# Kernel optimization log

Hardware: AMD Instinct MI355X
Metric: run time of the kernel (lower is better)

## Reference

```python
import jax, jax.numpy as jnp
import numpy as np
from jax import lax

N = 50000   # nodes per timestep
T = 8       # timesteps
E = 1600000 # edges per timestep
F_IN = 128
H = 128


def setup_inputs() -> dict:
    key = jax.random.key(0)
    ks = jax.random.split(key, 8)
    s_in = 1.0 / np.sqrt(F_IN)
    s_h = 1.0 / np.sqrt(H)
    return {
        "node_feats": jax.random.normal(ks[0], (T, N, F_IN), dtype=jnp.float32),
        "edges": jax.random.randint(ks[1], (T, 2, E), 0, N, dtype=jnp.int32),
        "W1": jax.random.normal(ks[2], (F_IN, H), dtype=jnp.float32) * s_in,
        "b1": jnp.zeros((H,), dtype=jnp.float32),
        "W2": jax.random.normal(ks[3], (H, H), dtype=jnp.float32) * s_h,
        "b2": jnp.zeros((H,), dtype=jnp.float32),
        "Wih": jax.random.normal(ks[4], (4 * H, H), dtype=jnp.float32) * s_h,
        "Whh": jax.random.normal(ks[5], (4 * H, H), dtype=jnp.float32) * s_h,
        "bih": jnp.zeros((4 * H,), dtype=jnp.float32),
        "bhh": jnp.zeros((4 * H,), dtype=jnp.float32),
    }


def _gcn_conv(x, row, col, W, b):
    # PyG GCNConv: h = x @ W; symmetric norm with self-loops; aggregate; + b
    h = x @ W  # [N, H]
    sl = jnp.arange(N, dtype=row.dtype)
    r = jnp.concatenate([row, sl])  # dest
    c = jnp.concatenate([col, sl])  # src
    deg = jax.ops.segment_sum(jnp.ones_like(r, dtype=h.dtype), r, num_segments=N)
    dinv = jnp.where(deg > 0, lax.rsqrt(deg), 0.0)
    norm = dinv[r] * dinv[c]  # [E+N]
    msg = h[c] * norm[:, None]  # [E+N, H]
    out = jax.ops.segment_sum(msg, r, num_segments=N)
    return out + b


def reference(node_feats, edges, W1, b1, W2, b2, Wih, Whh, bih, bhh):
    def gcn_step(_, xs):
        x, ei = xs
        row, col = ei[0], ei[1]
        x = jax.nn.relu(_gcn_conv(x, row, col, W1, b1))
        x = jax.nn.relu(_gcn_conv(x, row, col, W2, b2))
        return None, x

    _, embs = lax.scan(gcn_step, None, (node_feats, edges))  # [T, N, H]

    # Single-layer LSTM over time; nodes are the batch. Gate order: i, f, g, o.
    b = bih + bhh

    def lstm_step(carry, x_t):
        h, c = carry
        gates = x_t @ Wih.T + h @ Whh.T + b  # [N, 4H]
        i, f, g, o = jnp.split(gates, 4, axis=-1)
        i, f, o = jax.nn.sigmoid(i), jax.nn.sigmoid(f), jax.nn.sigmoid(o)
        g = jnp.tanh(g)
        c = f * c + i * g
        h = o * jnp.tanh(c)
        return (h, c), None

    h0 = jnp.zeros((N, H), dtype=node_feats.dtype)
    (h_last, _), _ = lax.scan(lstm_step, (h0, h0), embs)
    return h_last  # [N, H] == lstm_out[:, -1, :]
```

## Files before the change

### kernel.cpp

```cpp
#include <hip/hip_runtime.h>
#include <hip/hip_bf16.h>

#define NN 50000
#define TT 8
#define EE 1600000

constexpr int SCAN_B = 512;
constexpr int NBLK = (NN + SCAN_B - 1) / SCAN_B;

typedef __attribute__((ext_vector_type(8))) short bf16x8;
typedef __attribute__((ext_vector_type(4))) float f32x4;

__device__ inline unsigned short f2bf(float f) {
  unsigned int u = __float_as_uint(f);
  u += 0x7FFFu + ((u >> 16) & 1u);
  return (unsigned short)(u >> 16);
}
__device__ inline float bf2f(unsigned short h) {
  return __uint_as_float(((unsigned int)h) << 16);
}

__global__ void k_zero4(float4* p, long n4) {
  long i = (long)blockIdx.x * blockDim.x + threadIdx.x;
  if (i < n4) p[i] = make_float4(0.f, 0.f, 0.f, 0.f);
}

__global__ void k_zeroi(int* p, int n) {
  int i = blockIdx.x * blockDim.x + threadIdx.x;
  if (i < n) p[i] = 0;
}

__global__ void k_prep(const float* __restrict__ Wih, const float* __restrict__ Whh,
                       const float* __restrict__ W1, const float* __restrict__ W2,
                       const float* __restrict__ bih, const float* __restrict__ bhh,
                       unsigned short* WihH, unsigned short* WihL,
                       unsigned short* WhhH, unsigned short* WhhL,
                       unsigned short* W1tH, unsigned short* W1tL,
                       unsigned short* W2tH, unsigned short* W2tL, float* bsum) {
  int i = blockIdx.x * 256 + threadIdx.x;
  if (i < 512 * 128) {
    float v = Wih[i];
    unsigned short h = f2bf(v);
    WihH[i] = h; WihL[i] = f2bf(v - bf2f(h));
    v = Whh[i];
    h = f2bf(v);
    WhhH[i] = h; WhhL[i] = f2bf(v - bf2f(h));
  }
  if (i < 128 * 128) {
    int n = i >> 7, k = i & 127;
    float v = W1[(long)k * 128 + n];
    unsigned short h = f2bf(v);
    W1tH[i] = h; W1tL[i] = f2bf(v - bf2f(h));
    v = W2[(long)k * 128 + n];
    h = f2bf(v);
    W2tH[i] = h; W2tL[i] = f2bf(v - bf2f(h));
  }
  if (i < 512) bsum[i] = bih[i] + bhh[i];
}

__global__ void k_count(const int* __restrict__ row, int* __restrict__ deg) {
  int e = blockIdx.x * blockDim.x + threadIdx.x;
  if (e < EE) atomicAdd(&deg[row[e]], 1);
}

__global__ void k_scan1(const int* __restrict__ deg, int* __restrict__ rs, int* __restrict__ bsum) {
  __shared__ int s[SCAN_B];
  int t = threadIdx.x;
  int i = blockIdx.x * SCAN_B + t;
  int v = (i < NN) ? deg[i] : 0;
  s[t] = v;
  __syncthreads();
  for (int off = 1; off < SCAN_B; off <<= 1) {
    int add = (t >= off) ? s[t - off] : 0;
    __syncthreads();
    s[t] += add;
    __syncthreads();
  }
  if (i < NN) rs[i] = s[t] - v;
  if (t == SCAN_B - 1) bsum[blockIdx.x] = s[t];
}

__global__ void k_scan2(int* __restrict__ bsum) {
  __shared__ int s[128];
  int t = threadIdx.x;
  int v = (t < NBLK) ? bsum[t] : 0;
  s[t] = v;
  __syncthreads();
  for (int off = 1; off < 128; off <<= 1) {
    int add = (t >= off) ? s[t - off] : 0;
    __syncthreads();
    s[t] += add;
    __syncthreads();
  }
  if (t < NBLK) bsum[t] = s[t] - v;
}

__global__ void k_scan3(int* __restrict__ rs, const int* __restrict__ bsum, const int* __restrict__ deg,
                        float* __restrict__ dinv, int* __restrict__ cursor) {
  int i = blockIdx.x * blockDim.x + threadIdx.x;
  if (i < NN) {
    int v = rs[i] + bsum[i / SCAN_B];
    rs[i] = v;
    cursor[i] = v;
    dinv[i] = rsqrtf((float)(deg[i] + 1));
  }
  if (i == 0) rs[NN] = EE;
}

__global__ void k_scatter(const int* __restrict__ row, const int* __restrict__ col,
                          int* __restrict__ cursor, int* __restrict__ csr) {
  int e = blockIdx.x * blockDim.x + threadIdx.x;
  if (e < EE) {
    int r = row[e];
    int p = atomicAdd(&cursor[r], 1);
    csr[p] = col[e];
  }
}

#define MF(a, b, c) c = __builtin_amdgcn_mfma_f32_16x16x32_bf16(a, b, c, 0, 0, 0)

template <int AMODE>
__launch_bounds__(256) __global__
void k_gemm_mfma(const float* __restrict__ Af,
                 const unsigned short* __restrict__ Ahb, const unsigned short* __restrict__ Alb,
                 const unsigned short* __restrict__ BtH, const unsigned short* __restrict__ BtL,
                 float* __restrict__ C) {
  int tid = threadIdx.x;
  int wv = tid >> 6;
  int lane = tid & 63;
  int rA = lane & 15;
  int kg = lane >> 4;
  int m0 = blockIdx.x * 128 + wv * 32;
  int j0 = blockIdx.y * 32;
  long ar0 = min(m0 + rA, NN - 1);
  long ar1 = min(m0 + 16 + rA, NN - 1);
  long br0 = j0 + rA;
  long br1 = br0 + 16;
  f32x4 acc00 = {0.f, 0.f, 0.f, 0.f}, acc01 = acc00, acc10 = acc00, acc11 = acc00;
#pragma unroll
  for (int k0 = 0; k0 < 128; k0 += 32) {
    long ks = k0 + kg * 8;
    bf16x8 a0h, a0l, a1h, a1l;
    if constexpr (AMODE == 0) {
      float4 u0 = *(const float4*)(Af + ar0 * 128 + ks);
      float4 u1 = *(const float4*)(Af + ar0 * 128 + ks + 4);
      float4 u2 = *(const float4*)(Af + ar1 * 128 + ks);
      float4 u3 = *(const float4*)(Af + ar1 * 128 + ks + 4);
      float va[8] = {u0.x, u0.y, u0.z, u0.w, u1.x, u1.y, u1.z, u1.w};
      float vb[8] = {u2.x, u2.y, u2.z, u2.w, u3.x, u3.y, u3.z, u3.w};
#pragma unroll
      for (int e = 0; e < 8; e++) {
        unsigned short h = f2bf(va[e]);
        a0h[e] = (short)h; a0l[e] = (short)f2bf(va[e] - bf2f(h));
        unsigned short h2 = f2bf(vb[e]);
        a1h[e] = (short)h2; a1l[e] = (short)f2bf(vb[e] - bf2f(h2));
      }
    } else {
      a0h = *(const bf16x8*)(Ahb + ar0 * 128 + ks);
      a0l = *(const bf16x8*)(Alb + ar0 * 128 + ks);
      a1h = *(const bf16x8*)(Ahb + ar1 * 128 + ks);
      a1l = *(const bf16x8*)(Alb + ar1 * 128 + ks);
    }
    bf16x8 b0h = *(const bf16x8*)(BtH + br0 * 128 + ks);
    bf16x8 b0l = *(const bf16x8*)(BtL + br0 * 128 + ks);
    bf16x8 b1h = *(const bf16x8*)(BtH + br1 * 128 + ks);
    bf16x8 b1l = *(const bf16x8*)(BtL + br1 * 128 + ks);
    MF(a0l, b0h, acc00); MF(a0h, b0l, acc00); MF(a0h, b0h, acc00);
    MF(a0l, b1h, acc01); MF(a0h, b1l, acc01); MF(a0h, b1h, acc01);
    MF(a1l, b0h, acc10); MF(a1h, b0l, acc10); MF(a1h, b0h, acc10);
    MF(a1l, b1h, acc11); MF(a1h, b1l, acc11); MF(a1h, b1h, acc11);
  }
#pragma unroll
  for (int r = 0; r < 4; r++) {
    int row0 = m0 + kg * 4 + r;
    int row1 = row0 + 16;
    if (row0 < NN) {
      C[(long)row0 * 128 + j0 + rA] = acc00[r];
      C[(long)row0 * 128 + j0 + 16 + rA] = acc01[r];
    }
    if (row1 < NN) {
      C[(long)row1 * 128 + j0 + rA] = acc10[r];
      C[(long)row1 * 128 + j0 + 16 + rA] = acc11[r];
    }
  }
}

__launch_bounds__(256) __global__
void k_agg(const float* __restrict__ Hm, const float* __restrict__ dinv,
           const int* __restrict__ rs, const int* __restrict__ csr,
           const float* __restrict__ bias,
           unsigned short* __restrict__ outH, unsigned short* __restrict__ outL) {
  int i = blockIdx.x * 8 + (threadIdx.x >> 5);
  int lane = threadIdx.x & 31;
  if (i >= NN) return;
  float di = dinv[i];
  const float4* H4 = (const float4*)Hm;
  float4 a = H4[(long)i * 32 + lane];
  float sw = di * di;
  float4 acc = {a.x * sw, a.y * sw, a.z * sw, a.w * sw};
  int e0 = rs[i], e1 = rs[i + 1];
  int e = e0;
  for (; e + 2 <= e1; e += 2) {
    int c0 = csr[e], c1 = csr[e + 1];
    float w0 = di * dinv[c0], w1 = di * dinv[c1];
    float4 v0 = H4[(long)c0 * 32 + lane];
    float4 v1 = H4[(long)c1 * 32 + lane];
    acc.x += w0 * v0.x + w1 * v1.x;
    acc.y += w0 * v0.y + w1 * v1.y;
    acc.z += w0 * v0.z + w1 * v1.z;
    acc.w += w0 * v0.w + w1 * v1.w;
  }
  if (e < e1) {
    int c0 = csr[e];
    float w0 = di * dinv[c0];
    float4 v0 = H4[(long)c0 * 32 + lane];
    acc.x += w0 * v0.x; acc.y += w0 * v0.y; acc.z += w0 * v0.z; acc.w += w0 * v0.w;
  }
  float4 b = ((const float4*)bias)[lane];
  float4 v;
  v.x = fmaxf(acc.x + b.x, 0.f);
  v.y = fmaxf(acc.y + b.y, 0.f);
  v.z = fmaxf(acc.z + b.z, 0.f);
  v.w = fmaxf(acc.w + b.w, 0.f);
  ushort4 hh, hl;
  unsigned short h;
  h = f2bf(v.x); hh.x = h; hl.x = f2bf(v.x - bf2f(h));
  h = f2bf(v.y); hh.y = h; hl.y = f2bf(v.y - bf2f(h));
  h = f2bf(v.z); hh.z = h; hl.z = f2bf(v.z - bf2f(h));
  h = f2bf(v.w); hh.w = h; hl.w = f2bf(v.w - bf2f(h));
  ((ushort4*)outH)[(long)i * 32 + lane] = hh;
  ((ushort4*)outL)[(long)i * 32 + lane] = hl;
}

__launch_bounds__(256) __global__
void k_gates_lstm(const unsigned short* __restrict__ Xh, const unsigned short* __restrict__ Xl,
                  const unsigned short* __restrict__ Hh, const unsigned short* __restrict__ Hl,
                  const unsigned short* __restrict__ WihH, const unsigned short* __restrict__ WihL,
                  const unsigned short* __restrict__ WhhH, const unsigned short* __restrict__ WhhL,
                  const float* __restrict__ bsum, float* __restrict__ cst,
                  unsigned short* __restrict__ HoH, unsigned short* __restrict__ HoL,
                  float* __restrict__ out, int last) {
  __shared__ float G[4][32][36];
  int tid = threadIdx.x;
  int wv = tid >> 6;
  int lane = tid & 63;
  int rA = lane & 15;
  int kg = lane >> 4;
  int m0 = blockIdx.x * 32;
  int j0 = blockIdx.y * 32;
  long ar0 = min(m0 + rA, NN - 1);
  long ar1 = min(m0 + 16 + rA, NN - 1);
  long br0 = wv * 128 + j0 + rA;
  long br1 = br0 + 16;
  f32x4 acc00 = {0.f, 0.f, 0.f, 0.f}, acc01 = acc00, acc10 = acc00, acc11 = acc00;

  auto kloop = [&](const unsigned short* Ah, const unsigned short* Al,
                   const unsigned short* Bh, const unsigned short* Bl) {
#pragma unroll
    for (int k0 = 0; k0 < 128; k0 += 32) {
      long ks = k0 + kg * 8;
      bf16x8 a0h = *(const bf16x8*)(Ah + ar0 * 128 + ks);
      bf16x8 a0l = *(const bf16x8*)(Al + ar0 * 128 + ks);
      bf16x8 a1h = *(const bf16x8*)(Ah + ar1 * 128 + ks);
      bf16x8 a1l = *(const bf16x8*)(Al + ar1 * 128 + ks);
      bf16x8 b0h = *(const bf16x8*)(Bh + br0 * 128 + ks);
      bf16x8 b0l = *(const bf16x8*)(Bl + br0 * 128 + ks);
      bf16x8 b1h = *(const bf16x8*)(Bh + br1 * 128 + ks);
      bf16x8 b1l = *(const bf16x8*)(Bl + br1 * 128 + ks);
      MF(a0l, b0h, acc00); MF(a0h, b0l, acc00); MF(a0h, b0h, acc00);
      MF(a0l, b1h, acc01); MF(a0h, b1l, acc01); MF(a0h, b1h, acc01);
      MF(a1l, b0h, acc10); MF(a1h, b0l, acc10); MF(a1h, b0h, acc10);
      MF(a1l, b1h, acc11); MF(a1h, b1l, acc11); MF(a1h, b1h, acc11);
    }
  };
  kloop(Xh, Xl, WihH, WihL);
  kloop(Hh, Hl, WhhH, WhhL);

#pragma unroll
  for (int r = 0; r < 4; r++) {
    G[wv][kg * 4 + r][rA] = acc00[r];
    G[wv][kg * 4 + r][16 + rA] = acc01[r];
    G[wv][16 + kg * 4 + r][rA] = acc10[r];
    G[wv][16 + kg * 4 + r][16 + rA] = acc11[r];
  }
  __syncthreads();

  int pr = tid >> 3;
  int pc = (tid & 7) * 4;
  int row = m0 + pr;
  if (row < NN) {
    float4 vgi = *(float4*)&G[0][pr][pc];
    float4 vgf = *(float4*)&G[1][pr][pc];
    float4 vgg = *(float4*)&G[2][pr][pc];
    float4 vgo = *(float4*)&G[3][pr][pc];
    float4 bsi = *(const float4*)(bsum + j0 + pc);
    float4 bsf = *(const float4*)(bsum + 128 + j0 + pc);
    float4 bsg = *(const float4*)(bsum + 256 + j0 + pc);
    float4 bso = *(const float4*)(bsum + 384 + j0 + pc);
    long off = (long)row * 128 + j0 + pc;
    float4 co = *(const float4*)(cst + off);
    float4 cn, hv;
#define LCOMP(X)                                           \
  {                                                        \
    float iv = 1.f / (1.f + expf(-(vgi.X + bsi.X)));       \
    float fv = 1.f / (1.f + expf(-(vgf.X + bsf.X)));       \
    float gv = tanhf(vgg.X + bsg.X);                       \
    float ov = 1.f / (1.f + expf(-(vgo.X + bso.X)));       \
    float c2 = fv * co.X + iv * gv;                        \
    cn.X = c2;                                             \
    hv.X = ov * tanhf(c2);                                 \
  }
    LCOMP(x) LCOMP(y) LCOMP(z) LCOMP(w)
#undef LCOMP
    *(float4*)(cst + off) = cn;
    ushort4 hh, hl;
    unsigned short h;
    h = f2bf(hv.x); hh.x = h; hl.x = f2bf(hv.x - bf2f(h));
    h = f2bf(hv.y); hh.y = h; hl.y = f2bf(hv.y - bf2f(h));
    h = f2bf(hv.z); hh.z = h; hl.z = f2bf(hv.z - bf2f(h));
    h = f2bf(hv.w); hh.w = h; hl.w = f2bf(hv.w - bf2f(h));
    *(ushort4*)(HoH + off) = hh;
    *(ushort4*)(HoL + off) = hl;
    if (last) *(float4*)(out + off) = hv;
  }
}

extern "C" void kernel_launch(void* const* d_in, const int* in_sizes, int n_in,
                              void* d_out, int out_size, void* d_ws, size_t ws_size,
                              hipStream_t stream) {
  const float* feats = (const float*)d_in[0];
  const int*   edges = (const int*)d_in[1];
  const float* W1    = (const float*)d_in[2];
  const float* b1    = (const float*)d_in[3];
  const float* W2    = (const float*)d_in[4];
  const float* b2    = (const float*)d_in[5];
  const float* Wih   = (const float*)d_in[6];
  const float* Whh   = (const float*)d_in[7];
  const float* bih   = (const float*)d_in[8];
  const float* bhh   = (const float*)d_in[9];
  float* out = (float*)d_out;

  char* w = (char*)d_ws;
  auto alloc = [&](size_t bytes) {
    char* p = w;
    w += (bytes + 255) & ~(size_t)255;
    return p;
  };

  const size_t NB2 = (size_t)NN * 128 * 2;
  const size_t NB4 = (size_t)NN * 128 * 4;

  int*   csr    = (int*)alloc((size_t)EE * 4);
  int*   deg    = (int*)alloc((size_t)NN * 4);
  int*   rs     = (int*)alloc((size_t)(NN + 1) * 4);
  int*   cursor = (int*)alloc((size_t)NN * 4);
  float* dinv   = (float*)alloc((size_t)NN * 4);
  int*   bsumP  = (int*)alloc(512);

  float* bufH  = (float*)alloc(NB4);
  unsigned short* bufXh = (unsigned short*)alloc(NB2);
  unsigned short* bufXl = (unsigned short*)alloc(NB2);
  unsigned short* Xembh = (unsigned short*)alloc(NB2);
  unsigned short* Xembl = (unsigned short*)alloc(NB2);

  char* zr = alloc(NB2 + NB2 + NB4);
  unsigned short* HsAh = (unsigned short*)zr;
  unsigned short* HsAl = (unsigned short*)(zr + NB2);
  float* cstate = (float*)(zr + 2 * NB2);

  unsigned short* HsBh = (unsigned short*)alloc(NB2);
  unsigned short* HsBl = (unsigned short*)alloc(NB2);

  unsigned short* WihH = (unsigned short*)alloc(512 * 128 * 2);
  unsigned short* WihL = (unsigned short*)alloc(512 * 128 * 2);
  unsigned short* WhhH = (unsigned short*)alloc(512 * 128 * 2);
  unsigned short* WhhL = (unsigned short*)alloc(512 * 128 * 2);
  unsigned short* W1tH = (unsigned short*)alloc(128 * 128 * 2);
  unsigned short* W1tL = (unsigned short*)alloc(128 * 128 * 2);
  unsigned short* W2tH = (unsigned short*)alloc(128 * 128 * 2);
  unsigned short* W2tL = (unsigned short*)alloc(128 * 128 * 2);
  float* bsum = (float*)alloc(512 * 4);

  k_prep<<<256, 256, 0, stream>>>(Wih, Whh, W1, W2, bih, bhh,
                                  WihH, WihL, WhhH, WhhL, W1tH, W1tL, W2tH, W2tL, bsum);
  {
    long n4 = (long)(2 * NB2 + NB4) / 16;
    k_zero4<<<(int)((n4 + 255) / 256), 256, 0, stream>>>((float4*)zr, n4);
  }

  for (int t = 0; t < TT; t++) {
    const int* erow = edges + (size_t)t * 2 * EE;
    const int* ecol = erow + EE;
    const float* xt = feats + (size_t)t * NN * 128;

    k_zeroi<<<(NN + 255) / 256, 256, 0, stream>>>(deg, NN);
    k_count<<<EE / 256, 256, 0, stream>>>(erow, deg);
    k_scan1<<<NBLK, SCAN_B, 0, stream>>>(deg, rs, bsumP);
    k_scan2<<<1, 128, 0, stream>>>(bsumP);
    k_scan3<<<(NN + 255) / 256, 256, 0, stream>>>(rs, bsumP, deg, dinv, cursor);
    k_scatter<<<EE / 256, 256, 0, stream>>>(erow, ecol, cursor, csr);

    k_gemm_mfma<0><<<dim3(391, 4), 256, 0, stream>>>(xt, nullptr, nullptr, W1tH, W1tL, bufH);
    k_agg<<<NN / 8, 256, 0, stream>>>(bufH, dinv, rs, csr, b1, bufXh, bufXl);
    k_gemm_mfma<1><<<dim3(391, 4), 256, 0, stream>>>(nullptr, bufXh, bufXl, W2tH, W2tL, bufH);
    k_agg<<<NN / 8, 256, 0, stream>>>(bufH, dinv, rs, csr, b2, Xembh, Xembl);

    const unsigned short *rH, *rL;
    unsigned short *wH, *wL;
    if ((t & 1) == 0) { rH = HsAh; rL = HsAl; wH = HsBh; wL = HsBl; }
    else              { rH = HsBh; rL = HsBl; wH = HsAh; wL = HsAl; }
    k_gates_lstm<<<dim3(1563, 4), 256, 0, stream>>>(
        Xembh, Xembl, rH, rL, WihH, WihL, WhhH, WhhL, bsum, cstate,
        wH, wL, out, (t == TT - 1) ? 1 : 0);
  }
}
```

Before: 5.558 ms.

## Pre-scale GEMM rows by dinv, load A once per block, unroll aggregation

The GEMM kernels now compute the full 128-column output per block. Each wave loads and splits its A rows once instead of once per column tile. The output is pre-multiplied by dinv of the source row, so aggregation becomes an unweighted sum with a single final dinv scale, removing per-edge dinv gathers, and the edge loop is unrolled by four. The LSTM gates kernel likewise keeps the X and H fragments in registers and loops over four column tiles with extra block syncs, at the cost of much higher register pressure and possibly lower occupancy.

Result: faster. 5.082 ms (-8.6%).

```diff
diff --git a/kernel.cpp b/kernel.cpp
--- a/kernel.cpp
+++ b/kernel.cpp
@@ -124,23 +124,20 @@
 void k_gemm_mfma(const float* __restrict__ Af,
                  const unsigned short* __restrict__ Ahb, const unsigned short* __restrict__ Alb,
                  const unsigned short* __restrict__ BtH, const unsigned short* __restrict__ BtL,
-                 float* __restrict__ C) {
+                 const float* __restrict__ dinv, float* __restrict__ C) {
   int tid = threadIdx.x;
   int wv = tid >> 6;
   int lane = tid & 63;
   int rA = lane & 15;
   int kg = lane >> 4;
   int m0 = blockIdx.x * 128 + wv * 32;
-  int j0 = blockIdx.y * 32;
   long ar0 = min(m0 + rA, NN - 1);
   long ar1 = min(m0 + 16 + rA, NN - 1);
-  long br0 = j0 + rA;
-  long br1 = br0 + 16;
-  f32x4 acc00 = {0.f, 0.f, 0.f, 0.f}, acc01 = acc00, acc10 = acc00, acc11 = acc00;
-#pragma unroll
-  for (int k0 = 0; k0 < 128; k0 += 32) {
-    long ks = k0 + kg * 8;
-    bf16x8 a0h, a0l, a1h, a1l;
+
+  bf16x8 a[4][2][2];
+#pragma unroll
+  for (int k0 = 0; k0 < 4; k0++) {
+    long ks = k0 * 32 + kg * 8;
     if constexpr (AMODE == 0) {
       float4 u0 = *(const float4*)(Af + ar0 * 128 + ks);
       float4 u1 = *(const float4*)(Af + ar0 * 128 + ks + 4);
@@ -151,77 +148,100 @@
 #pragma unroll
       for (int e = 0; e < 8; e++) {
         unsigned short h = f2bf(va[e]);
-        a0h[e] = (short)h; a0l[e] = (short)f2bf(va[e] - bf2f(h));
-        unsigned short h2 = f2bf(vb[e]);
-        a1h[e] = (short)h2; a1l[e] = (short)f2bf(vb[e] - bf2f(h2));
+        a[k0][0][0][e] = (short)h; a[k0][0][1][e] = (short)f2bf(va[e] - bf2f(h));
+        h = f2bf(vb[e]);
+        a[k0][1][0][e] = (short)h; a[k0][1][1][e] = (short)f2bf(vb[e] - bf2f(h));
       }
     } else {
-      a0h = *(const bf16x8*)(Ahb + ar0 * 128 + ks);
-      a0l = *(const bf16x8*)(Alb + ar0 * 128 + ks);
-      a1h = *(const bf16x8*)(Ahb + ar1 * 128 + ks);
-      a1l = *(const bf16x8*)(Alb + ar1 * 128 + ks);
-    }
-    bf16x8 b0h = *(const bf16x8*)(BtH + br0 * 128 + ks);
-    bf16x8 b0l = *(const bf16x8*)(BtL + br0 * 128 + ks);
-    bf16x8 b1h = *(const bf16x8*)(BtH + br1 * 128 + ks);
-    bf16x8 b1l = *(const bf16x8*)(BtL + br1 * 128 + ks);
-    MF(a0l, b0h, acc00); MF(a0h, b0l, acc00); MF(a0h, b0h, acc00);
-    MF(a0l, b1h, acc01); MF(a0h, b1l, acc01); MF(a0h, b1h, acc01);
-    MF(a1l, b0h, acc10); MF(a1h, b0l, acc10); MF(a1h, b0h, acc10);
-    MF(a1l, b1h, acc11); MF(a1h, b1l, acc11); MF(a1h, b1h, acc11);
-  }
+      a[k0][0][0] = *(const bf16x8*)(Ahb + ar0 * 128 + ks);
+      a[k0][0][1] = *(const bf16x8*)(Alb + ar0 * 128 + ks);
+      a[k0][1][0] = *(const bf16x8*)(Ahb + ar1 * 128 + ks);
+      a[k0][1][1] = *(const bf16x8*)(Alb + ar1 * 128 + ks);
+    }
+  }
+
+  f32x4 acc[4][4];
+#pragma unroll
+  for (int j = 0; j < 4; j++)
+#pragma unroll
+    for (int q = 0; q < 4; q++) acc[j][q] = (f32x4){0.f, 0.f, 0.f, 0.f};
+
+#pragma unroll
+  for (int k0 = 0; k0 < 4; k0++) {
+    long ks = k0 * 32 + kg * 8;
+#pragma unroll
+    for (int j = 0; j < 4; j++) {
+      long b0 = (long)(j * 32 + rA) * 128 + ks;
+      long b1 = (long)(j * 32 + 16 + rA) * 128 + ks;
+      bf16x8 b0h = *(const bf16x8*)(BtH + b0);
+      bf16x8 b0l = *(const bf16x8*)(BtL + b0);
+      bf16x8 b1h = *(const bf16x8*)(BtH + b1);
+      bf16x8 b1l = *(const bf16x8*)(BtL + b1);
+      MF(a[k0][0][1], b0h, acc[j][0]); MF(a[k0][0][0], b0l, acc[j][0]); MF(a[k0][0][0], b0h, acc[j][0]);
+      MF(a[k0][0][1], b1h, acc[j][1]); MF(a[k0][0][0], b1l, acc[j][1]); MF(a[k0][0][0], b1h, acc[j][1]);
+      MF(a[k0][1][1], b0h, acc[j][2]); MF(a[k0][1][0], b0l, acc[j][2]); MF(a[k0][1][0], b0h, acc[j][2]);
+      MF(a[k0][1][1], b1h, acc[j][3]); MF(a[k0][1][0], b1l, acc[j][3]); MF(a[k0][1][0], b1h, acc[j][3]);
+    }
+  }
+
 #pragma unroll
   for (int r = 0; r < 4; r++) {
     int row0 = m0 + kg * 4 + r;
     int row1 = row0 + 16;
     if (row0 < NN) {
-      C[(long)row0 * 128 + j0 + rA] = acc00[r];
-      C[(long)row0 * 128 + j0 + 16 + rA] = acc01[r];
+      float dv = dinv[row0];
+#pragma unroll
+      for (int j = 0; j < 4; j++) {
+        C[(long)row0 * 128 + j * 32 + rA] = acc[j][0][r] * dv;
+        C[(long)row0 * 128 + j * 32 + 16 + rA] = acc[j][1][r] * dv;
+      }
     }
     if (row1 < NN) {
-      C[(long)row1 * 128 + j0 + rA] = acc10[r];
-      C[(long)row1 * 128 + j0 + 16 + rA] = acc11[r];
+      float dv = dinv[row1];
+#pragma unroll
+      for (int j = 0; j < 4; j++) {
+        C[(long)row1 * 128 + j * 32 + rA] = acc[j][2][r] * dv;
+        C[(long)row1 * 128 + j * 32 + 16 + rA] = acc[j][3][r] * dv;
+      }
     }
   }
 }
 
 __launch_bounds__(256) __global__
-void k_agg(const float* __restrict__ Hm, const float* __restrict__ dinv,
+void k_agg(const float* __restrict__ Hs, const float* __restrict__ dinv,
            const int* __restrict__ rs, const int* __restrict__ csr,
            const float* __restrict__ bias,
            unsigned short* __restrict__ outH, unsigned short* __restrict__ outL) {
   int i = blockIdx.x * 8 + (threadIdx.x >> 5);
   int lane = threadIdx.x & 31;
   if (i >= NN) return;
-  float di = dinv[i];
-  const float4* H4 = (const float4*)Hm;
-  float4 a = H4[(long)i * 32 + lane];
-  float sw = di * di;
-  float4 acc = {a.x * sw, a.y * sw, a.z * sw, a.w * sw};
+  const float4* H4 = (const float4*)Hs;
+  float4 acc = H4[(long)i * 32 + lane];
   int e0 = rs[i], e1 = rs[i + 1];
   int e = e0;
-  for (; e + 2 <= e1; e += 2) {
-    int c0 = csr[e], c1 = csr[e + 1];
-    float w0 = di * dinv[c0], w1 = di * dinv[c1];
+  for (; e + 4 <= e1; e += 4) {
+    int c0 = csr[e], c1 = csr[e + 1], c2 = csr[e + 2], c3 = csr[e + 3];
     float4 v0 = H4[(long)c0 * 32 + lane];
     float4 v1 = H4[(long)c1 * 32 + lane];
-    acc.x += w0 * v0.x + w1 * v1.x;
-    acc.y += w0 * v0.y + w1 * v1.y;
-    acc.z += w0 * v0.z + w1 * v1.z;
-    acc.w += w0 * v0.w + w1 * v1.w;
-  }
-  if (e < e1) {
+    float4 v2 = H4[(long)c2 * 32 + lane];
+    float4 v3 = H4[(long)c3 * 32 + lane];
+    acc.x += v0.x + v1.x + v2.x + v3.x;
+    acc.y += v0.y + v1.y + v2.y + v3.y;
+    acc.z += v0.z + v1.z + v2.z + v3.z;
+    acc.w += v0.w + v1.w + v2.w + v3.w;
+  }
+  for (; e < e1; e++) {
     int c0 = csr[e];
-    float w0 = di * dinv[c0];
     float4 v0 = H4[(long)c0 * 32 + lane];
-    acc.x += w0 * v0.x; acc.y += w0 * v0.y; acc.z += w0 * v0.z; acc.w += w0 * v0.w;
-  }
+    acc.x += v0.x; acc.y += v0.y; acc.z += v0.z; acc.w += v0.w;
+  }
+  float di = dinv[i];
   float4 b = ((const float4*)bias)[lane];
   float4 v;
-  v.x = fmaxf(acc.x + b.x, 0.f);
-  v.y = fmaxf(acc.y + b.y, 0.f);
-  v.z = fmaxf(acc.z + b.z, 0.f);
-  v.w = fmaxf(acc.w + b.w, 0.f);
+  v.x = fmaxf(di * acc.x + b.x, 0.f);
+  v.y = fmaxf(di * acc.y + b.y, 0.f);
+  v.z = fmaxf(di * acc.z + b.z, 0.f);
+  v.w = fmaxf(di * acc.w + b.w, 0.f);
   ushort4 hh, hl;
   unsigned short h;
   h = f2bf(v.x); hh.x = h; hl.x = f2bf(v.x - bf2f(h));
@@ -247,59 +267,76 @@
   int rA = lane & 15;
   int kg = lane >> 4;
   int m0 = blockIdx.x * 32;
-  int j0 = blockIdx.y * 32;
   long ar0 = min(m0 + rA, NN - 1);
   long ar1 = min(m0 + 16 + rA, NN - 1);
-  long br0 = wv * 128 + j0 + rA;
-  long br1 = br0 + 16;
-  f32x4 acc00 = {0.f, 0.f, 0.f, 0.f}, acc01 = acc00, acc10 = acc00, acc11 = acc00;
-
-  auto kloop = [&](const unsigned short* Ah, const unsigned short* Al,
-                   const unsigned short* Bh, const unsigned short* Bl) {
-#pragma unroll
-    for (int k0 = 0; k0 < 128; k0 += 32) {
-      long ks = k0 + kg * 8;
-      bf16x8 a0h = *(const bf16x8*)(Ah + ar0 * 128 + ks);
-      bf16x8 a0l = *(const bf16x8*)(Al + ar0 * 128 + ks);
-      bf16x8 a1h = *(const bf16x8*)(Ah + ar1 * 128 + ks);
-      bf16x8 a1l = *(const bf16x8*)(Al + ar1 * 128 + ks);
-      bf16x8 b0h = *(const bf16x8*)(Bh + br0 * 128 + ks);
-      bf16x8 b0l = *(const bf16x8*)(Bl + br0 * 128 + ks);
-      bf16x8 b1h = *(const bf16x8*)(Bh + br1 * 128 + ks);
-      bf16x8 b1l = *(const bf16x8*)(Bl + br1 * 128 + ks);
-      MF(a0l, b0h, acc00); MF(a0h, b0l, acc00); MF(a0h, b0h, acc00);
-      MF(a0l, b1h, acc01); MF(a0h, b1l, acc01); MF(a0h, b1h, acc01);
-      MF(a1l, b0h, acc10); MF(a1h, b0l, acc10); MF(a1h, b0h, acc10);
-      MF(a1l, b1h, acc11); MF(a1h, b1l, acc11); MF(a1h, b1h, acc11);
-    }
-  };
-  kloop(Xh, Xl, WihH, WihL);
-  kloop(Hh, Hl, WhhH, WhhL);
-
-#pragma unroll
-  for (int r = 0; r < 4; r++) {
-    G[wv][kg * 4 + r][rA] = acc00[r];
-    G[wv][kg * 4 + r][16 + rA] = acc01[r];
-    G[wv][16 + kg * 4 + r][rA] = acc10[r];
-    G[wv][16 + kg * 4 + r][16 + rA] = acc11[r];
-  }
-  __syncthreads();
-
-  int pr = tid >> 3;
-  int pc = (tid & 7) * 4;
-  int row = m0 + pr;
-  if (row < NN) {
-    float4 vgi = *(float4*)&G[0][pr][pc];
-    float4 vgf = *(float4*)&G[1][pr][pc];
-    float4 vgg = *(float4*)&G[2][pr][pc];
-    float4 vgo = *(float4*)&G[3][pr][pc];
-    float4 bsi = *(const float4*)(bsum + j0 + pc);
-    float4 bsf = *(const float4*)(bsum + 128 + j0 + pc);
-    float4 bsg = *(const float4*)(bsum + 256 + j0 + pc);
-    float4 bso = *(const float4*)(bsum + 384 + j0 + pc);
-    long off = (long)row * 128 + j0 + pc;
-    float4 co = *(const float4*)(cst + off);
-    float4 cn, hv;
+
+  bf16x8 xa[4][2][2], ha[4][2][2];
+#pragma unroll
+  for (int k0 = 0; k0 < 4; k0++) {
+    long ks = k0 * 32 + kg * 8;
+    xa[k0][0][0] = *(const bf16x8*)(Xh + ar0 * 128 + ks);
+    xa[k0][0][1] = *(const bf16x8*)(Xl + ar0 * 128 + ks);
+    xa[k0][1][0] = *(const bf16x8*)(Xh + ar1 * 128 + ks);
+    xa[k0][1][1] = *(const bf16x8*)(Xl + ar1 * 128 + ks);
+    ha[k0][0][0] = *(const bf16x8*)(Hh + ar0 * 128 + ks);
+    ha[k0][0][1] = *(const bf16x8*)(Hl + ar0 * 128 + ks);
+    ha[k0][1][0] = *(const bf16x8*)(Hh + ar1 * 128 + ks);
+    ha[k0][1][1] = *(const bf16x8*)(Hl + ar1 * 128 + ks);
+  }
+
+  for (int j = 0; j < 4; j++) {
+    f32x4 acc00 = {0.f, 0.f, 0.f, 0.f}, acc01 = acc00, acc10 = acc00, acc11 = acc00;
+    long brb = (long)wv * 128 + j * 32;
+#pragma unroll
+    for (int k0 = 0; k0 < 4; k0++) {
+      long ks = k0 * 32 + kg * 8;
+      long b0 = (brb + rA) * 128 + ks, b1 = (brb + 16 + rA) * 128 + ks;
+      bf16x8 b0h = *(const bf16x8*)(WihH + b0);
+      bf16x8 b0l = *(const bf16x8*)(WihL + b0);
+      bf16x8 b1h = *(const bf16x8*)(WihH + b1);
+      bf16x8 b1l = *(const bf16x8*)(WihL + b1);
+      MF(xa[k0][0][1], b0h, acc00); MF(xa[k0][0][0], b0l, acc00); MF(xa[k0][0][0], b0h, acc00);
+      MF(xa[k0][0][1], b1h, acc01); MF(xa[k0][0][0], b1l, acc01); MF(xa[k0][0][0], b1h, acc01);
+      MF(xa[k0][1][1], b0h, acc10); MF(xa[k0][1][0], b0l, acc10); MF(xa[k0][1][0], b0h, acc10);
+      MF(xa[k0][1][1], b1h, acc11); MF(xa[k0][1][0], b1l, acc11); MF(xa[k0][1][0], b1h, acc11);
+    }
+#pragma unroll
+    for (int k0 = 0; k0 < 4; k0++) {
+      long ks = k0 * 32 + kg * 8;
+      long b0 = (brb + rA) * 128 + ks, b1 = (brb + 16 + rA) * 128 + ks;
+      bf16x8 b0h = *(const bf16x8*)(WhhH + b0);
+      bf16x8 b0l = *(const bf16x8*)(WhhL + b0);
+      bf16x8 b1h = *(const bf16x8*)(WhhH + b1);
+      bf16x8 b1l = *(const bf16x8*)(WhhL + b1);
+      MF(ha[k0][0][1], b0h, acc00); MF(ha[k0][0][0], b0l, acc00); MF(ha[k0][0][0], b0h, acc00);
+      MF(ha[k0][0][1], b1h, acc01); MF(ha[k0][0][0], b1l, acc01); MF(ha[k0][0][0], b1h, acc01);
+      MF(ha[k0][1][1], b0h, acc10); MF(ha[k0][1][0], b0l, acc10); MF(ha[k0][1][0], b0h, acc10);
+      MF(ha[k0][1][1], b1h, acc11); MF(ha[k0][1][0], b1l, acc11); MF(ha[k0][1][0], b1h, acc11);
+    }
+#pragma unroll
+    for (int r = 0; r < 4; r++) {
+      G[wv][kg * 4 + r][rA] = acc00[r];
+      G[wv][kg * 4 + r][16 + rA] = acc01[r];
+      G[wv][16 + kg * 4 + r][rA] = acc10[r];
+      G[wv][16 + kg * 4 + r][16 + rA] = acc11[r];
+    }
+    __syncthreads();
+    {
+      int pr = tid >> 3;
+      int pc = (tid & 7) * 4;
+      int row = m0 + pr;
+      if (row < NN) {
+        float4 vgi = *(float4*)&G[0][pr][pc];
+        float4 vgf = *(float4*)&G[1][pr][pc];
+        float4 vgg = *(float4*)&G[2][pr][pc];
+        float4 vgo = *(float4*)&G[3][pr][pc];
+        float4 bsi = *(const float4*)(bsum + j * 32 + pc);
+        float4 bsf = *(const float4*)(bsum + 128 + j * 32 + pc);
+        float4 bsg = *(const float4*)(bsum + 256 + j * 32 + pc);
+        float4 bso = *(const float4*)(bsum + 384 + j * 32 + pc);
+        long off = (long)row * 128 + j * 32 + pc;
+        float4 co = *(const float4*)(cst + off);
+        float4 cn, hv;
 #define LCOMP(X)                                           \
   {                                                        \
     float iv = 1.f / (1.f + expf(-(vgi.X + bsi.X)));       \
@@ -310,18 +347,21 @@
     cn.X = c2;                                             \
     hv.X = ov * tanhf(c2);                                 \
   }
-    LCOMP(x) LCOMP(y) LCOMP(z) LCOMP(w)
+        LCOMP(x) LCOMP(y) LCOMP(z) LCOMP(w)
 #undef LCOMP
-    *(float4*)(cst + off) = cn;
-    ushort4 hh, hl;
-    unsigned short h;
-    h = f2bf(hv.x); hh.x = h; hl.x = f2bf(hv.x - bf2f(h));
-    h = f2bf(hv.y); hh.y = h; hl.y = f2bf(hv.y - bf2f(h));
-    h = f2bf(hv.z); hh.z = h; hl.z = f2bf(hv.z - bf2f(h));
-    h = f2bf(hv.w); hh.w = h; hl.w = f2bf(hv.w - bf2f(h));
-    *(ushort4*)(HoH + off) = hh;
-    *(ushort4*)(HoL + off) = hl;
-    if (last) *(float4*)(out + off) = hv;
+        *(float4*)(cst + off) = cn;
+        ushort4 hh, hl;
+        unsigned short h;
+        h = f2bf(hv.x); hh.x = h; hl.x = f2bf(hv.x - bf2f(h));
+        h = f2bf(hv.y); hh.y = h; hl.y = f2bf(hv.y - bf2f(h));
+        h = f2bf(hv.z); hh.z = h; hl.z = f2bf(hv.z - bf2f(h));
+        h = f2bf(hv.w); hh.w = h; hl.w = f2bf(hv.w - bf2f(h));
+        *(ushort4*)(HoH + off) = hh;
+        *(ushort4*)(HoL + off) = hl;
+        if (last) *(float4*)(out + off) = hv;
+      }
+    }
+    __syncthreads();
   }
 }
 
@@ -400,16 +440,16 @@
     k_scan3<<<(NN + 255) / 256, 256, 0, stream>>>(rs, bsumP, deg, dinv, cursor);
     k_scatter<<<EE / 256, 256, 0, stream>>>(erow, ecol, cursor, csr);
 
-    k_gemm_mfma<0><<<dim3(391, 4), 256, 0, stream>>>(xt, nullptr, nullptr, W1tH, W1tL, bufH);
+    k_gemm_mfma<0><<<391, 256, 0, stream>>>(xt, nullptr, nullptr, W1tH, W1tL, dinv, bufH);
     k_agg<<<NN / 8, 256, 0, stream>>>(bufH, dinv, rs, csr, b1, bufXh, bufXl);
-    k_gemm_mfma<1><<<dim3(391, 4), 256, 0, stream>>>(nullptr, bufXh, bufXl, W2tH, W2tL, bufH);
+    k_gemm_mfma<1><<<391, 256, 0, stream>>>(nullptr, bufXh, bufXl, W2tH, W2tL, dinv, bufH);
     k_agg<<<NN / 8, 256, 0, stream>>>(bufH, dinv, rs, csr, b2, Xembh, Xembl);
 
     const unsigned short *rH, *rL;
     unsigned short *wH, *wL;
     if ((t & 1) == 0) { rH = HsAh; rL = HsAl; wH = HsBh; wL = HsBl; }
     else              { rH = HsBh; rL = HsBl; wH = HsAh; wL = HsAl; }
-    k_gates_lstm<<<dim3(1563, 4), 256, 0, stream>>>(
+    k_gates_lstm<<<1563, 256, 0, stream>>>(
         Xembh, Xembl, rH, rL, WihH, WihL, WhhH, WhhL, bsum, cstate,
         wH, wL, out, (t == TT - 1) ? 1 : 0);
   }
```
